# Optimization experiments

Measured on AMD Instinct MI355X. Metric: run time of the kernel, lower is better.

## Reference

```python
import jax, jax.numpy as jnp
import numpy as np

B, T, D, H, TW = 4, 4096, 2560, 10, 4
C_CONST = 8.0  # RG-LRU 'c' constant from the paper/code


def setup_inputs() -> dict:
    key = jax.random.key(0)
    ks = jax.random.split(key, 8)
    s = 1.0 / np.sqrt(D)  # variance_scaling fan_in
    Dh = D // H
    return dict(
        x=jax.random.normal(ks[0], (B, T, D), jnp.float32),
        segment_pos=jnp.tile(jnp.arange(T, dtype=jnp.int32), (B, 1)),
        Wy=(jax.random.normal(ks[1], (D, D), jnp.float32) * s),
        by=jnp.zeros((D,), jnp.float32),
        Wx=(jax.random.normal(ks[2], (D, D), jnp.float32) * s),
        bx=jnp.zeros((D,), jnp.float32),
        conv_w=(jax.random.normal(ks[3], (TW, D), jnp.float32) * (1.0 / np.sqrt(TW))),
        conv_b=jnp.zeros((D,), jnp.float32),
        a_param=jax.random.uniform(ks[4], (D,), jnp.float32, minval=-4.0, maxval=-3.0),
        ig_w=(jax.random.normal(ks[5], (H, Dh, Dh), jnp.float32) * (1.0 / np.sqrt(Dh))),
        ig_b=jnp.zeros((H, Dh), jnp.float32),
        ag_w=(jax.random.normal(ks[6], (H, Dh, Dh), jnp.float32) * (1.0 / np.sqrt(Dh))),
        ag_b=jnp.zeros((H, Dh), jnp.float32),
        Wo=(jax.random.normal(ks[7], (D, D), jnp.float32) * s),
        bo=jnp.zeros((D,), jnp.float32),
    )


def _block_diag_linear(x, w, b):
    # x: [B,T,D]; w: [H,Dh,Dh]; b: [H,Dh]
    Bb, Tt, Dd = x.shape
    Hh = w.shape[0]
    xh = x.reshape(Bb, Tt, Hh, -1)
    yh = jnp.einsum('bthd,hdk->bthk', xh, w) + b
    return yh.reshape(Bb, Tt, Dd)


def _forward(x, segment_pos, Wy, by, Wx, bx, conv_w, conv_b, a_param,
             ig_w, ig_b, ag_w, ag_b, Wo, bo):
    # Gate branch: dense + gelu
    y = jax.nn.gelu(x @ Wy + by)
    # Main branch: dense
    xb = x @ Wx + bx
    # Causal depthwise conv1d (left zero pad), w[TW-1] multiplies current token
    tw = conv_w.shape[0]
    seq = xb.shape[1]
    xp = jnp.pad(xb, ((0, 0), (tw - 1, 0), (0, 0)))
    conv = conv_b[None, None]
    for i in range(tw):
        conv = conv + conv_w[i][None, None] * xp[:, i:i + seq]
    # RG-LRU
    reset = (segment_pos == 0)[..., None]  # [B,T,1]
    gate_x = jax.nn.sigmoid(_block_diag_linear(conv, ig_w, ig_b))
    gate_a = jax.nn.sigmoid(_block_diag_linear(conv, ag_w, ag_b))
    log_a = -C_CONST * gate_a * jax.nn.softplus(a_param)  # [B,T,D]
    a = jnp.exp(log_a)
    multiplier = jnp.sqrt(1.0 - jnp.exp(2.0 * log_a))
    multiplier = jnp.where(reset, 1.0, multiplier)
    norm_x = conv * gate_x * multiplier
    a = jnp.where(reset, 0.0, a)
    # diagonal linear scan: h_t = a_t * h_{t-1} + norm_x_t
    def step(h, inp):
        a_t, x_t = inp
        h = a_t * h + x_t
        return h, h
    h0 = jnp.zeros((x.shape[0], a.shape[-1]), a.dtype)
    _, hs = jax.lax.scan(step, h0, (jnp.swapaxes(a, 0, 1), jnp.swapaxes(norm_x, 0, 1)))
    h = jnp.swapaxes(hs, 0, 1)  # [B,T,D]
    # elementwise gate and output projection
    return (h * y) @ Wo + bo


def reference(x, segment_pos, Wy, by, Wx, bx, conv_w, conv_b, a_param,
              ig_w, ig_b, ag_w, ag_b, Wo, bo):
    return _forward(x, segment_pos, Wy, by, Wx, bx, conv_w, conv_b, a_param,
                    ig_w, ig_b, ag_w, ag_b, Wo, bo)
```

## Files before the change

### kernel.cpp

```cpp
#include <hip/hip_runtime.h>

#define D_DIM 2560
#define T_DIM 4096
#define B_DIM 4
#define H_DIM 10
#define DH 256
#define TW_DIM 4
#define M_DIM (B_DIM * T_DIM)
#define CHUNKS 64
#define TC (T_DIM / CHUNKS)

typedef _Float16 f16;
typedef __attribute__((ext_vector_type(8))) _Float16 f16x8;
typedef __attribute__((ext_vector_type(4))) _Float16 f16x4;
typedef __attribute__((ext_vector_type(2))) _Float16 f16x2;
typedef __attribute__((ext_vector_type(4))) float f32x4;
typedef __attribute__((ext_vector_type(2))) float f32x2;

__global__ void cvt_f16_kernel(const float* __restrict__ in, f16* __restrict__ out, long n4) {
  long i = (long)blockIdx.x * blockDim.x + threadIdx.x;
  if (i >= n4) return;
  f32x4 v = ((const f32x4*)in)[i];
  f16x4 o;
  o[0] = (f16)v[0]; o[1] = (f16)v[1]; o[2] = (f16)v[2]; o[3] = (f16)v[3];
  ((f16x4*)out)[i] = o;
}

__global__ void transpose_cvt3_kernel(const float* __restrict__ s0, const float* __restrict__ s1,
                                      const float* __restrict__ s2, f16* __restrict__ out,
                                      int R, int C) {
  __shared__ float tile[32][33];
  const int z = blockIdx.z;
  const float* in = (z == 0) ? s0 : ((z == 1) ? s1 : s2);
  out += (long)z * R * C;
  int c0 = blockIdx.x * 32, r0 = blockIdx.y * 32;
  int tx = threadIdx.x, ty = threadIdx.y;
  for (int i = ty; i < 32; i += 8)
    tile[i][tx] = in[(long)(r0 + i) * C + (c0 + tx)];
  __syncthreads();
  for (int i = ty; i < 32; i += 8)
    out[(long)(c0 + i) * R + (r0 + tx)] = (f16)tile[tx][i];
}

__global__ void transpose_cvt2_kernel(const float* __restrict__ sa, const float* __restrict__ sb,
                                      f16* __restrict__ out, int R, int C, int half) {
  __shared__ float tile[32][33];
  const int z = blockIdx.z;
  const float* in = (z < half) ? (sa + (long)z * R * C) : (sb + (long)(z - half) * R * C);
  out += (long)z * R * C;
  int c0 = blockIdx.x * 32, r0 = blockIdx.y * 32;
  int tx = threadIdx.x, ty = threadIdx.y;
  for (int i = ty; i < 32; i += 8)
    tile[i][tx] = in[(long)(r0 + i) * C + (c0 + tx)];
  __syncthreads();
  for (int i = ty; i < 32; i += 8)
    out[(long)(c0 + i) * R + (r0 + tx)] = (f16)tile[tx][i];
}

__device__ __forceinline__ void async_cp16(const void* g, void* l) {
  __builtin_amdgcn_global_load_lds(
      (const __attribute__((address_space(1))) unsigned int*)g,
      (__attribute__((address_space(3))) unsigned int*)l, 16, 0, 0);
}

__device__ __forceinline__ float fast_sigmoid(float v) {
  return 1.f / (1.f + __expf(-v));
}

#define BM2 256
#define BN2 256
#define BK2 32

template<int ACT, int OUT16>
__global__ __launch_bounds__(512, 2)
void gemm256_kernel(const f16* __restrict__ A, long ldA,
                    const f16* __restrict__ Bt, long ldB,
                    const float* __restrict__ bias,
                    void* __restrict__ Cv, long ldC, int K) {
  __shared__ __attribute__((aligned(16))) f16 sm[4 * 16384];
  const int tid = threadIdx.x;
  const int wave = tid >> 6;
  const int lane = tid & 63;
  const int wm = wave >> 2;
  const int wn = wave & 3;
  const long bm = (long)blockIdx.y * BM2;
  const long bn = (long)blockIdx.x * BN2;

  const int sRow = wave * 16 + (lane >> 2);
  const int sChunk = (lane & 3) ^ ((lane >> 2) & 3);
  const int sOff = sChunk * 8;
  const f16* pA0 = A + (bm + sRow) * ldA + sOff;
  const f16* pA1 = pA0 + 128 * ldA;
  const f16* pB0 = Bt + (bn + sRow) * ldB + sOff;
  const f16* pB1 = pB0 + 128 * ldB;
  const int wOff = wave * 512;

  const int quad = lane >> 4, l16 = lane & 15;
  const int rswz = (quad ^ (l16 & 3)) * 8;
  const int aRowBase = (wm * 128 + l16) * BK2 + rswz;
  const int bRowBase = (wn * 64 + l16) * BK2 + rswz;

  f32x4 acc[8][4];
#pragma unroll
  for (int i = 0; i < 8; ++i)
#pragma unroll
    for (int j = 0; j < 4; ++j) {
      acc[i][j][0] = 0.f; acc[i][j][1] = 0.f; acc[i][j][2] = 0.f; acc[i][j][3] = 0.f;
    }

  const int NT = K / BK2;

#pragma unroll
  for (int p = 0; p < 3; ++p) {
    f16* dst = sm + p * 16384;
    const int kp = (p < NT ? p : NT - 1) * BK2;
    async_cp16(pA0 + kp, dst + wOff);
    async_cp16(pA1 + kp, dst + 4096 + wOff);
    async_cp16(pB0 + kp, dst + 8192 + wOff);
    async_cp16(pB1 + kp, dst + 12288 + wOff);
  }
  asm volatile("s_waitcnt vmcnt(8)" ::: "memory");
  __builtin_amdgcn_s_barrier();

#pragma unroll 4
  for (int t = 0; t < NT; ++t) {
    const f16* As = sm + (t & 3) * 16384;
    const f16* Bs = As + 8192;
    const int kp = (t + 3 < NT ? t + 3 : NT - 1) * BK2;
    f16* dst = sm + ((t + 3) & 3) * 16384;

    f16x8 af0[4], bf[4];
#pragma unroll
    for (int i = 0; i < 4; ++i) af0[i] = *(const f16x8*)&As[aRowBase + i * 16 * BK2];
#pragma unroll
    for (int j = 0; j < 4; ++j) bf[j]  = *(const f16x8*)&Bs[bRowBase + j * 16 * BK2];
    async_cp16(pA0 + kp, dst + wOff);
    async_cp16(pA1 + kp, dst + 4096 + wOff);
    __builtin_amdgcn_s_setprio(1);
#pragma unroll
    for (int i = 0; i < 4; ++i)
#pragma unroll
      for (int j = 0; j < 4; ++j)
        acc[i][j] = __builtin_amdgcn_mfma_f32_16x16x32_f16(af0[i], bf[j], acc[i][j], 0, 0, 0);
    __builtin_amdgcn_s_setprio(0);

    f16x8 af1[4];
#pragma unroll
    for (int i = 0; i < 4; ++i) af1[i] = *(const f16x8*)&As[aRowBase + (64 + i * 16) * BK2];
    async_cp16(pB0 + kp, dst + 8192 + wOff);
    async_cp16(pB1 + kp, dst + 12288 + wOff);
    __builtin_amdgcn_s_setprio(1);
#pragma unroll
    for (int i = 0; i < 4; ++i)
#pragma unroll
      for (int j = 0; j < 4; ++j)
        acc[4 + i][j] = __builtin_amdgcn_mfma_f32_16x16x32_f16(af1[i], bf[j], acc[4 + i][j], 0, 0, 0);
    __builtin_amdgcn_s_setprio(0);

    asm volatile("s_waitcnt vmcnt(8)" ::: "memory");
    __builtin_amdgcn_s_barrier();
  }

#pragma unroll
  for (int i = 0; i < 8; ++i) {
    const long row0 = bm + wm * 128 + i * 16 + quad * 4;
#pragma unroll
    for (int j = 0; j < 4; ++j) {
      const long colIn = bn + wn * 64 + j * 16 + l16;
      const float bv = bias[colIn];
#pragma unroll
      for (int r = 0; r < 4; ++r) {
        const long row = row0 + r;
        float v = acc[i][j][r] + bv;
        if (ACT == 1) {
          const float u = v;
          const float tt = 0.7978845608028654f * (u + 0.044715f * u * u * u);
          v = u * fast_sigmoid(2.f * tt);
        }
        const long cidx = row * ldC + colIn;
        if (OUT16) ((f16*)Cv)[cidx] = (f16)v;
        else       ((float*)Cv)[cidx] = v;
      }
    }
  }
}

#define BM 128
#define BN 128
#define BK 32

template<int ACT, int OUT16>
__global__ __launch_bounds__(256, 2)
void gemm_kernel(const f16* __restrict__ A, long ldA, long zA,
                 const f16* __restrict__ Bt, long zB,
                 const float* __restrict__ bias, long zBias,
                 void* __restrict__ Cv, long ldC, long zC, int K,
                 const f16* __restrict__ cX, const f16* __restrict__ gX,
                 const float* __restrict__ apar, const int* __restrict__ segp,
                 f16* __restrict__ nxOut) {
  __shared__ __attribute__((aligned(16))) f16 As[BM * BK];
  __shared__ __attribute__((aligned(16))) f16 Bs[BN * BK];
  const int tid = threadIdx.x;
  const int wave = tid >> 6;
  const int lane = tid & 63;
  const int wm = wave >> 1, wn = wave & 1;
  const long bm = (long)blockIdx.y * BM;
  const long bn = (long)blockIdx.x * BN;
  const int z = blockIdx.z;
  A += (long)z * zA;
  Bt += (long)z * zB;
  bias += (long)z * zBias;
  const long cColOff = (long)z * zC;

  const int sRow = wave * 32 + (lane >> 2);
  const int sCol = (((lane & 3) ^ (sRow & 3)) * 8);
  const f16* gA = A + (bm + sRow) * ldA + sCol;
  const f16* gB = Bt + (bn + sRow) * (long)K + sCol;
  f16* lA = As + wave * 1024;
  f16* lB = Bs + wave * 1024;

  f32x4 acc[4][4];
#pragma unroll
  for (int i = 0; i < 4; ++i)
#pragma unroll
    for (int j = 0; j < 4; ++j) {
      acc[i][j][0] = 0.f; acc[i][j][1] = 0.f; acc[i][j][2] = 0.f; acc[i][j][3] = 0.f;
    }

  const int quad = lane >> 4, l16 = lane & 15;
  const int rswz = (quad ^ (l16 & 3)) * 8;

  for (int k0 = 0; k0 < K; k0 += BK) {
    async_cp16(gA, lA);
    async_cp16(gA + 16 * ldA, lA + 512);
    async_cp16(gB, lB);
    async_cp16(gB + 16 * (long)K, lB + 512);
    gA += BK; gB += BK;
    __syncthreads();
    f16x8 af[4], bf[4];
#pragma unroll
    for (int i = 0; i < 4; ++i) {
      af[i] = *(const f16x8*)&As[(wm * 64 + i * 16 + l16) * BK + rswz];
      bf[i] = *(const f16x8*)&Bs[(wn * 64 + i * 16 + l16) * BK + rswz];
    }
#pragma unroll
    for (int i = 0; i < 4; ++i)
#pragma unroll
      for (int j = 0; j < 4; ++j)
        acc[i][j] = __builtin_amdgcn_mfma_f32_16x16x32_f16(af[i], bf[j], acc[i][j], 0, 0, 0);
    __syncthreads();
  }

#pragma unroll
  for (int i = 0; i < 4; ++i) {
    const long row0 = bm + wm * 64 + i * 16 + quad * 4;
#pragma unroll
    for (int j = 0; j < 4; ++j) {
      const long colIn = bn + wn * 64 + j * 16 + l16;
      const long colG = cColOff + colIn;
      const float bv = bias[colIn];
      float sp = 0.f;
      if (ACT == 3) sp = log1pf(__expf(apar[colG]));
#pragma unroll
      for (int r = 0; r < 4; ++r) {
        const long row = row0 + r;
        float v = acc[i][j][r] + bv;
        if (ACT == 1) {
          const float u = v;
          const float t = 0.7978845608028654f * (u + 0.044715f * u * u * u);
          v = u * fast_sigmoid(2.f * t);
        } else if (ACT == 2) {
          v = fast_sigmoid(v);
        }
        const long cidx = row * ldC + colG;
        if (ACT == 3) {
          const float ga = fast_sigmoid(v);
          const float log_a = -8.f * ga * sp;
          float a = __expf(log_a);
          float mult = sqrtf(fmaxf(1.f - __expf(2.f * log_a), 0.f));
          if (segp[row] == 0) { a = 0.f; mult = 1.f; }
          const float nx = (float)cX[cidx] * (float)gX[cidx] * mult;
          ((f16*)Cv)[cidx] = (f16)a;
          nxOut[cidx] = (f16)nx;
        } else if (OUT16) {
          ((f16*)Cv)[cidx] = (f16)v;
        } else {
          ((float*)Cv)[cidx] = v;
        }
      }
    }
  }
}

__global__ void conv_kernel(const f16* __restrict__ xb, const float* __restrict__ cw,
                            const float* __restrict__ cb, f16* __restrict__ out) {
  const int d4 = blockIdx.x * 128 + threadIdx.x;
  const int t = blockIdx.y;
  const int b = blockIdx.z;
  const long idx4 = ((long)b * T_DIM + t) * (D_DIM / 4) + d4;
  f32x4 acc = ((const f32x4*)cb)[d4];
#pragma unroll
  for (int i = 0; i < TW_DIM; ++i) {
    const int tt = t - (TW_DIM - 1) + i;
    if (tt >= 0) {
      f16x4 xv = ((const f16x4*)xb)[idx4 + (long)(i - (TW_DIM - 1)) * (D_DIM / 4)];
      f32x4 w = ((const f32x4*)cw)[i * (D_DIM / 4) + d4];
      acc[0] += w[0] * (float)xv[0];
      acc[1] += w[1] * (float)xv[1];
      acc[2] += w[2] * (float)xv[2];
      acc[3] += w[3] * (float)xv[3];
    }
  }
  f16x4 o;
  o[0] = (f16)acc[0]; o[1] = (f16)acc[1]; o[2] = (f16)acc[2]; o[3] = (f16)acc[3];
  ((f16x4*)out)[idx4] = o;
}

__global__ void scanA_kernel(const f16* __restrict__ a16, const f16* __restrict__ nx16,
                             float* __restrict__ Ac, float* __restrict__ Sc) {
  const int d2 = blockIdx.x * 256 + threadIdx.x;
  const int c = blockIdx.y;
  const int b = blockIdx.z;
  long base2 = ((long)b * T_DIM + (long)c * TC) * (D_DIM / 2) + d2;
  float Ap0 = 1.f, Ap1 = 1.f, S0 = 0.f, S1 = 0.f;
  for (int t = 0; t < TC; ++t) {
    f16x2 av = ((const f16x2*)a16)[base2];
    f16x2 xv = ((const f16x2*)nx16)[base2];
    S0 = (float)av[0] * S0 + (float)xv[0];
    S1 = (float)av[1] * S1 + (float)xv[1];
    Ap0 *= (float)av[0];
    Ap1 *= (float)av[1];
    base2 += D_DIM / 2;
  }
  const long cidx2 = ((long)b * CHUNKS + c) * (D_DIM / 2) + d2;
  f32x2 av_; av_[0] = Ap0; av_[1] = Ap1;
  f32x2 sv_; sv_[0] = S0; sv_[1] = S1;
  ((f32x2*)Ac)[cidx2] = av_;
  ((f32x2*)Sc)[cidx2] = sv_;
}

__global__ void scanB_kernel(const float* __restrict__ Ac, const float* __restrict__ Sc,
                             float* __restrict__ He) {
  const int d = blockIdx.x * 256 + threadIdx.x;
  const int b = blockIdx.z;
  float h = 0.f;
  for (int c = 0; c < CHUNKS; ++c) {
    const long cidx = ((long)b * CHUNKS + c) * D_DIM + d;
    He[cidx] = h;
    h = Ac[cidx] * h + Sc[cidx];
  }
}

__global__ void scanC_kernel(const f16* __restrict__ a16, const f16* __restrict__ nx16,
                             const float* __restrict__ He, const f16* __restrict__ y16,
                             f16* __restrict__ hy16) {
  const int d2 = blockIdx.x * 256 + threadIdx.x;
  const int c = blockIdx.y;
  const int b = blockIdx.z;
  long base2 = ((long)b * T_DIM + (long)c * TC) * (D_DIM / 2) + d2;
  f32x2 hv = ((const f32x2*)He)[((long)b * CHUNKS + c) * (D_DIM / 2) + d2];
  float h0 = hv[0], h1 = hv[1];
  for (int t = 0; t < TC; ++t) {
    f16x2 av = ((const f16x2*)a16)[base2];
    f16x2 xv = ((const f16x2*)nx16)[base2];
    f16x2 yv = ((const f16x2*)y16)[base2];
    h0 = (float)av[0] * h0 + (float)xv[0];
    h1 = (float)av[1] * h1 + (float)xv[1];
    f16x2 o;
    o[0] = (f16)(h0 * (float)yv[0]);
    o[1] = (f16)(h1 * (float)yv[1]);
    ((f16x2*)hy16)[base2] = o;
    base2 += D_DIM / 2;
  }
}

extern "C" void kernel_launch(void* const* d_in, const int* in_sizes, int n_in,
                              void* d_out, int out_size, void* d_ws, size_t ws_size,
                              hipStream_t stream) {
  const float* x   = (const float*)d_in[0];
  const int*   segp= (const int*)d_in[1];
  const float* Wy  = (const float*)d_in[2];
  const float* by  = (const float*)d_in[3];
  const float* Wx  = (const float*)d_in[4];
  const float* bx  = (const float*)d_in[5];
  const float* cw  = (const float*)d_in[6];
  const float* cb  = (const float*)d_in[7];
  const float* ap  = (const float*)d_in[8];
  const float* igw = (const float*)d_in[9];
  const float* igb = (const float*)d_in[10];
  const float* agw = (const float*)d_in[11];
  const float* agb = (const float*)d_in[12];
  const float* Wo  = (const float*)d_in[13];
  const float* bo  = (const float*)d_in[14];
  float* out = (float*)d_out;
  char* ws = (char*)d_ws;

  const long MD = (long)M_DIM * D_DIM;
  f16*   x16    = (f16*)(ws + 0);
  f16*   a16    = (f16*)(ws + 0);
  f16*   y16    = (f16*)(ws + MD * 2);
  f16*   xb2    = (f16*)(ws + MD * 4);
  f16*   gx16   = (f16*)(ws + MD * 4);
  f16*   hy16   = (f16*)(ws + MD * 4);
  f16*   conv16 = (f16*)(ws + MD * 6);
  f16*   nx16   = (f16*)(ws + MD * 8);
  long off = MD * 10;
  f16* Wt  = (f16*)(ws + off); off += 3L * D_DIM * D_DIM * 2;
  f16* igagt = (f16*)(ws + off); off += 20L * DH * DH * 2;
  float* Ac = (float*)(ws + off); off += (long)B_DIM * CHUNKS * D_DIM * 4;
  float* Sc = (float*)(ws + off); off += (long)B_DIM * CHUNKS * D_DIM * 4;
  float* He = (float*)(ws + off); off += (long)B_DIM * CHUNKS * D_DIM * 4;
  f16* Wyt = Wt;
  f16* Wxt = Wt + (long)D_DIM * D_DIM;
  f16* Wot = Wt + 2L * D_DIM * D_DIM;
  f16* igt = igagt;
  f16* agt = igagt + 10L * DH * DH;

  dim3 tb(32, 8);
  cvt_f16_kernel<<<dim3((unsigned)(MD / 4 / 256)), 256, 0, stream>>>(x, x16, MD / 4);
  transpose_cvt3_kernel<<<dim3(80, 80, 3), tb, 0, stream>>>(Wy, Wx, Wo, Wt, D_DIM, D_DIM);
  transpose_cvt2_kernel<<<dim3(8, 8, 20), tb, 0, stream>>>(igw, agw, igagt, DH, DH, 10);
  gemm256_kernel<1, 1><<<dim3(10, 64, 1), 512, 0, stream>>>(
      x16, D_DIM, Wyt, D_DIM, by, (void*)y16, D_DIM, D_DIM);
  gemm256_kernel<0, 1><<<dim3(10, 64, 1), 512, 0, stream>>>(
      x16, D_DIM, Wxt, D_DIM, bx, (void*)xb2, D_DIM, D_DIM);
  conv_kernel<<<dim3(5, 4096, 4), 128, 0, stream>>>(xb2, cw, cb, conv16);
  gemm_kernel<2, 1><<<dim3(2, 128, 10), 256, 0, stream>>>(
      conv16, D_DIM, DH, igt, (long)DH * DH, igb, DH, (void*)gx16, D_DIM, DH, DH,
      nullptr, nullptr, nullptr, nullptr, nullptr);
  gemm_kernel<3, 1><<<dim3(2, 128, 10), 256, 0, stream>>>(
      conv16, D_DIM, DH, agt, (long)DH * DH, agb, DH, (void*)a16, D_DIM, DH, DH,
      conv16, gx16, ap, segp, nx16);
  scanA_kernel<<<dim3(5, CHUNKS, 4), 256, 0, stream>>>(a16, nx16, Ac, Sc);
  scanB_kernel<<<dim3(10, 1, 4), 256, 0, stream>>>(Ac, Sc, He);
  scanC_kernel<<<dim3(5, CHUNKS, 4), 256, 0, stream>>>(a16, nx16, He, y16, hy16);
  gemm256_kernel<0, 0><<<dim3(10, 64, 1), 512, 0, stream>>>(
      hy16, D_DIM, Wot, D_DIM, bo, (void*)out, D_DIM, D_DIM);
}
```

Baseline: 1.475 ms.

## Fuse input and a-gate GEMMs, remap workgroups, and strengthen LDS swizzle

The two block-diagonal gate GEMMs become a single kernel that loads each conv tile once, accumulates both the input-gate and a-gate products, and computes a and normalized x directly in the epilogue. This removes the gx16 intermediate write and read and one full pass over conv16. The big GEMM also gets an interleaved workgroup-to-tile mapping meant to improve L2 locality, plus an extra XOR term in the LDS swizzle to reduce bank conflicts. The cost is higher register and LDS use in the fused kernel, which may lower occupancy.

```diff
diff --git a/kernel.cpp b/kernel.cpp
--- a/kernel.cpp
+++ b/kernel.cpp
@@ -83,11 +83,16 @@
   const int lane = tid & 63;
   const int wm = wave >> 2;
   const int wn = wave & 3;
-  const long bm = (long)blockIdx.y * BM2;
-  const long bn = (long)blockIdx.x * BN2;
+
+  const int nx_ = gridDim.x;
+  const int nwg = nx_ * gridDim.y;
+  int lid = blockIdx.y * nx_ + blockIdx.x;
+  lid = (lid & 7) * (nwg >> 3) + (lid >> 3);
+  const long bm = (long)(lid / nx_) * BM2;
+  const long bn = (long)(lid % nx_) * BN2;
 
   const int sRow = wave * 16 + (lane >> 2);
-  const int sChunk = (lane & 3) ^ ((lane >> 2) & 3);
+  const int sChunk = (lane & 3) ^ ((lane >> 2) & 3) ^ ((lane >> 4) & 3);
   const int sOff = sChunk * 8;
   const f16* pA0 = A + (bm + sRow) * ldA + sOff;
   const f16* pA1 = pA0 + 128 * ldA;
@@ -96,7 +101,7 @@
   const int wOff = wave * 512;
 
   const int quad = lane >> 4, l16 = lane & 15;
-  const int rswz = (quad ^ (l16 & 3)) * 8;
+  const int rswz = (quad ^ (l16 & 3) ^ ((l16 >> 2) & 3)) * 8;
   const int aRowBase = (wm * 128 + l16) * BK2 + rswz;
   const int bRowBase = (wn * 64 + l16) * BK2 + rswz;
 
@@ -189,17 +194,15 @@
 #define BN 128
 #define BK 32
 
-template<int ACT, int OUT16>
 __global__ __launch_bounds__(256, 2)
-void gemm_kernel(const f16* __restrict__ A, long ldA, long zA,
-                 const f16* __restrict__ Bt, long zB,
-                 const float* __restrict__ bias, long zBias,
-                 void* __restrict__ Cv, long ldC, long zC, int K,
-                 const f16* __restrict__ cX, const f16* __restrict__ gX,
-                 const float* __restrict__ apar, const int* __restrict__ segp,
-                 f16* __restrict__ nxOut) {
+void gemm_gates_kernel(const f16* __restrict__ A, long ldA,
+                       const f16* __restrict__ igt, const f16* __restrict__ agt,
+                       const float* __restrict__ igb, const float* __restrict__ agb,
+                       const float* __restrict__ apar, const int* __restrict__ segp,
+                       f16* __restrict__ aOut, f16* __restrict__ nxOut, int K) {
   __shared__ __attribute__((aligned(16))) f16 As[BM * BK];
-  __shared__ __attribute__((aligned(16))) f16 Bs[BN * BK];
+  __shared__ __attribute__((aligned(16))) f16 B1s[BN * BK];
+  __shared__ __attribute__((aligned(16))) f16 B2s[BN * BK];
   const int tid = threadIdx.x;
   const int wave = tid >> 6;
   const int lane = tid & 63;
@@ -207,47 +210,57 @@
   const long bm = (long)blockIdx.y * BM;
   const long bn = (long)blockIdx.x * BN;
   const int z = blockIdx.z;
-  A += (long)z * zA;
-  Bt += (long)z * zB;
-  bias += (long)z * zBias;
-  const long cColOff = (long)z * zC;
+  const f16* Az = A + (long)z * DH;
+  const f16* B1 = igt + (long)z * DH * DH;
+  const f16* B2 = agt + (long)z * DH * DH;
+  const float* b1 = igb + (long)z * DH;
+  const float* b2 = agb + (long)z * DH;
+  const long cColOff = (long)z * DH;
 
   const int sRow = wave * 32 + (lane >> 2);
-  const int sCol = (((lane & 3) ^ (sRow & 3)) * 8);
-  const f16* gA = A + (bm + sRow) * ldA + sCol;
-  const f16* gB = Bt + (bn + sRow) * (long)K + sCol;
+  const int sCol = ((lane & 3) ^ (sRow & 3) ^ ((sRow >> 2) & 3)) * 8;
+  const f16* gA = Az + (bm + sRow) * ldA + sCol;
+  const f16* gB1 = B1 + (bn + sRow) * (long)K + sCol;
+  const f16* gB2 = B2 + (bn + sRow) * (long)K + sCol;
   f16* lA = As + wave * 1024;
-  f16* lB = Bs + wave * 1024;
-
-  f32x4 acc[4][4];
+  f16* lB1 = B1s + wave * 1024;
+  f16* lB2 = B2s + wave * 1024;
+
+  f32x4 accI[4][4], accA[4][4];
 #pragma unroll
   for (int i = 0; i < 4; ++i)
 #pragma unroll
     for (int j = 0; j < 4; ++j) {
-      acc[i][j][0] = 0.f; acc[i][j][1] = 0.f; acc[i][j][2] = 0.f; acc[i][j][3] = 0.f;
+      accI[i][j][0] = 0.f; accI[i][j][1] = 0.f; accI[i][j][2] = 0.f; accI[i][j][3] = 0.f;
+      accA[i][j][0] = 0.f; accA[i][j][1] = 0.f; accA[i][j][2] = 0.f; accA[i][j][3] = 0.f;
     }
 
   const int quad = lane >> 4, l16 = lane & 15;
-  const int rswz = (quad ^ (l16 & 3)) * 8;
+  const int rswz = (quad ^ (l16 & 3) ^ ((l16 >> 2) & 3)) * 8;
 
   for (int k0 = 0; k0 < K; k0 += BK) {
     async_cp16(gA, lA);
     async_cp16(gA + 16 * ldA, lA + 512);
-    async_cp16(gB, lB);
-    async_cp16(gB + 16 * (long)K, lB + 512);
-    gA += BK; gB += BK;
+    async_cp16(gB1, lB1);
+    async_cp16(gB1 + 16 * (long)K, lB1 + 512);
+    async_cp16(gB2, lB2);
+    async_cp16(gB2 + 16 * (long)K, lB2 + 512);
+    gA += BK; gB1 += BK; gB2 += BK;
     __syncthreads();
-    f16x8 af[4], bf[4];
+    f16x8 af[4], bf1[4], bf2[4];
 #pragma unroll
     for (int i = 0; i < 4; ++i) {
-      af[i] = *(const f16x8*)&As[(wm * 64 + i * 16 + l16) * BK + rswz];
-      bf[i] = *(const f16x8*)&Bs[(wn * 64 + i * 16 + l16) * BK + rswz];
+      af[i]  = *(const f16x8*)&As[(wm * 64 + i * 16 + l16) * BK + rswz];
+      bf1[i] = *(const f16x8*)&B1s[(wn * 64 + i * 16 + l16) * BK + rswz];
+      bf2[i] = *(const f16x8*)&B2s[(wn * 64 + i * 16 + l16) * BK + rswz];
     }
 #pragma unroll
     for (int i = 0; i < 4; ++i)
 #pragma unroll
-      for (int j = 0; j < 4; ++j)
-        acc[i][j] = __builtin_amdgcn_mfma_f32_16x16x32_f16(af[i], bf[j], acc[i][j], 0, 0, 0);
+      for (int j = 0; j < 4; ++j) {
+        accI[i][j] = __builtin_amdgcn_mfma_f32_16x16x32_f16(af[i], bf1[j], accI[i][j], 0, 0, 0);
+        accA[i][j] = __builtin_amdgcn_mfma_f32_16x16x32_f16(af[i], bf2[j], accA[i][j], 0, 0, 0);
+      }
     __syncthreads();
   }
 
@@ -258,35 +271,22 @@
     for (int j = 0; j < 4; ++j) {
       const long colIn = bn + wn * 64 + j * 16 + l16;
       const long colG = cColOff + colIn;
-      const float bv = bias[colIn];
-      float sp = 0.f;
-      if (ACT == 3) sp = log1pf(__expf(apar[colG]));
+      const float bv1 = b1[colIn];
+      const float bv2 = b2[colIn];
+      const float sp = log1pf(__expf(apar[colG]));
 #pragma unroll
       for (int r = 0; r < 4; ++r) {
         const long row = row0 + r;
-        float v = acc[i][j][r] + bv;
-        if (ACT == 1) {
-          const float u = v;
-          const float t = 0.7978845608028654f * (u + 0.044715f * u * u * u);
-          v = u * fast_sigmoid(2.f * t);
-        } else if (ACT == 2) {
-          v = fast_sigmoid(v);
-        }
-        const long cidx = row * ldC + colG;
-        if (ACT == 3) {
-          const float ga = fast_sigmoid(v);
-          const float log_a = -8.f * ga * sp;
-          float a = __expf(log_a);
-          float mult = sqrtf(fmaxf(1.f - __expf(2.f * log_a), 0.f));
-          if (segp[row] == 0) { a = 0.f; mult = 1.f; }
-          const float nx = (float)cX[cidx] * (float)gX[cidx] * mult;
-          ((f16*)Cv)[cidx] = (f16)a;
-          nxOut[cidx] = (f16)nx;
-        } else if (OUT16) {
-          ((f16*)Cv)[cidx] = (f16)v;
-        } else {
-          ((float*)Cv)[cidx] = v;
-        }
+        const float gx = fast_sigmoid(accI[i][j][r] + bv1);
+        const float ga = fast_sigmoid(accA[i][j][r] + bv2);
+        const float log_a = -8.f * ga * sp;
+        float a = __expf(log_a);
+        float mult = sqrtf(fmaxf(1.f - __expf(2.f * log_a), 0.f));
+        if (segp[row] == 0) { a = 0.f; mult = 1.f; }
+        const long cidx = row * D_DIM + colG;
+        const float cv = (float)A[row * ldA + colG];
+        aOut[cidx] = (f16)a;
+        nxOut[cidx] = (f16)(cv * gx * mult);
       }
     }
   }
@@ -400,7 +400,6 @@
   f16*   a16    = (f16*)(ws + 0);
   f16*   y16    = (f16*)(ws + MD * 2);
   f16*   xb2    = (f16*)(ws + MD * 4);
-  f16*   gx16   = (f16*)(ws + MD * 4);
   f16*   hy16   = (f16*)(ws + MD * 4);
   f16*   conv16 = (f16*)(ws + MD * 6);
   f16*   nx16   = (f16*)(ws + MD * 8);
@@ -425,12 +424,8 @@
   gemm256_kernel<0, 1><<<dim3(10, 64, 1), 512, 0, stream>>>(
       x16, D_DIM, Wxt, D_DIM, bx, (void*)xb2, D_DIM, D_DIM);
   conv_kernel<<<dim3(5, 4096, 4), 128, 0, stream>>>(xb2, cw, cb, conv16);
-  gemm_kernel<2, 1><<<dim3(2, 128, 10), 256, 0, stream>>>(
-      conv16, D_DIM, DH, igt, (long)DH * DH, igb, DH, (void*)gx16, D_DIM, DH, DH,
-      nullptr, nullptr, nullptr, nullptr, nullptr);
-  gemm_kernel<3, 1><<<dim3(2, 128, 10), 256, 0, stream>>>(
-      conv16, D_DIM, DH, agt, (long)DH * DH, agb, DH, (void*)a16, D_DIM, DH, DH,
-      conv16, gx16, ap, segp, nx16);
+  gemm_gates_kernel<<<dim3(2, 128, 10), 256, 0, stream>>>(
+      conv16, D_DIM, igt, agt, igb, agb, ap, segp, a16, nx16, DH);
   scanA_kernel<<<dim3(5, CHUNKS, 4), 256, 0, stream>>>(a16, nx16, Ac, Sc);
   scanB_kernel<<<dim3(10, 1, 4), 256, 0, stream>>>(Ac, Sc, He);
   scanC_kernel<<<dim3(5, CHUNKS, 4), 256, 0, stream>>>(a16, nx16, He, y16, hy16);
```

New measurement: 1.358 ms. -8.0%, faster.
